# Kernel tuning notes

Hardware: AMD Instinct MI355X
Metric: run time of the kernel (lower is better)

Reference implementation:

```python
import jax, jax.numpy as jnp
import numpy as np

def setup_inputs() -> dict:
    key = jax.random.key(0)
    kS, kD = jax.random.split(key)
    B, Ls, Ld, d = 8, 2048, 2048, 1024
    S = jax.random.normal(kS, (B, Ls, d), dtype=jnp.float32)
    D = jax.random.normal(kD, (B, Ld, d), dtype=jnp.float32)
    return {"S": S, "D": D}

def reference(S, D):
    # scores_D: [B, Ld, Ls] = D @ S^T ; scores_S: [B, Ls, Ld] = S @ D^T
    attn_D = jax.nn.softmax(jnp.einsum('bld,bmd->blm', D, S), axis=-1)
    attn_S = jax.nn.softmax(jnp.einsum('bmd,bld->bml', S, D), axis=-1)
    co_D = D + jnp.einsum('blm,bmd->bld', attn_D, S)
    co_S = S + jnp.einsum('bml,bld->bmd', attn_S, D)
    return (co_D, co_S)
```

## Files before the change

### kernel.cpp

```cpp
#include <hip/hip_runtime.h>

typedef __attribute__((ext_vector_type(8))) _Float16 f16x8;
typedef __attribute__((ext_vector_type(16))) float f32x16;

#define B_    8
#define LSEQ  2048
#define DIM   1024
#define QBLK  64
#define KBLK  128
#define NKB   (LSEQ / KBLK)
#define NDC   (DIM / 128)
#define NBAND (DIM / 128)

#define TILE_US   16384
#define KIMG_US   ((size_t)2 * 8 * 16 * 8 * TILE_US)
#define WS_NEED   ((size_t)2 * KIMG_US * 2)

static __device__ __forceinline__ unsigned pk2(float a, float b) {
    return __builtin_bit_cast(unsigned, __builtin_amdgcn_cvt_pkrtz(a, b));
}

#define VMCNT(n) asm volatile("s_waitcnt vmcnt(" #n ")" ::: "memory")
#define BAR()    do { asm volatile("" ::: "memory"); __builtin_amdgcn_s_barrier(); \
                      asm volatile("" ::: "memory"); } while (0)

static __device__ __forceinline__ void gll16(const void* g, void* l) {
    __builtin_amdgcn_global_load_lds(
        (const __attribute__((address_space(1))) void*)g,
        (__attribute__((address_space(3))) void*)l, 16, 0, 0);
}

static __device__ __forceinline__ void issue32(const unsigned short* gt, unsigned short* lb, int w, int lane) {
    #pragma unroll
    for (int j = 0; j < 4; ++j) {
        const int off = (w * 4 + j) * 1024;
        gll16((const char*)gt + off + lane * 16, (char*)lb + off);
    }
}
static __device__ __forceinline__ void issue16(const unsigned short* gt, unsigned short* lb, int w, int lane) {
    #pragma unroll
    for (int j = 0; j < 2; ++j) {
        const int off = (w * 2 + j) * 1024;
        gll16((const char*)gt + off + lane * 16, (char*)lb + off);
    }
}

__global__ __launch_bounds__(256)
void prepass(const float* __restrict__ Sp, const float* __restrict__ Dp,
             unsigned short* __restrict__ Kimg, unsigned short* __restrict__ Vimg)
{
    const int blk = blockIdx.x;
    const int dc = blk & 7;
    const int kb = (blk >> 3) & 15;
    const int b  = (blk >> 7) & 7;
    const int m  = blk >> 10;
    const float* src = (m ? Dp : Sp) + ((size_t)b * LSEQ + kb * 128) * DIM + dc * 128;
    unsigned short* kt = Kimg + (size_t)((((m * 8 + b) * 16 + kb) * 8) + dc) * TILE_US;
    unsigned short* vt = Vimg + (size_t)((((m * 8 + b) * 8 + dc) * 16) + kb) * TILE_US;

    __shared__ unsigned short tile[128 * 132];
    const int t = threadIdx.x;

    #pragma unroll
    for (int i = 0; i < 16; ++i) {
        const int idx = t + i * 256;
        const int r = idx >> 5;
        const int c4 = (idx & 31) << 2;
        const float4 v = *(const float4*)(src + (size_t)r * DIM + c4);
        const unsigned lo = pk2(v.x, v.y), hi2 = pk2(v.z, v.w);
        *(uint2*)(kt + r * 128 + (c4 ^ ((r & 7) << 3))) = make_uint2(lo, hi2);
        *(uint2*)(&tile[r * 132 + c4]) = make_uint2(lo, hi2);
    }
    __syncthreads();
    #pragma unroll
    for (int i = 0; i < 32; ++i) {
        const int widx = t + i * 256;
        const int dcl = widx >> 6;
        const int wk  = widx & 63;
        const unsigned a  = tile[(wk * 2) * 132 + dcl];
        const unsigned bb = tile[(wk * 2 + 1) * 132 + dcl];
        ((unsigned*)vt)[dcl * 64 + (wk ^ ((dcl & 7) << 2))] = a | (bb << 16);
    }
}

__global__ __launch_bounds__(512, 2)
void coattn_main(const float* __restrict__ Sp, const float* __restrict__ Dp,
                 float* __restrict__ outp,
                 const unsigned short* __restrict__ Kimg,
                 const unsigned short* __restrict__ Vimg)
{
    const int s   = blockIdx.x;
    const int g   = (s & 7) | ((s >> 8) << 3);
    const int qb  = (s >> 3) & 31;
    const int dir = g >> 3;
    const int b   = g & 7;
    const int mat_k = dir;
    const int mat_q = 1 - dir;

    const float* Qg = (dir ? Sp : Dp) + (size_t)b * LSEQ * DIM;
    float* Og = outp + (size_t)dir * ((size_t)B_ * LSEQ * DIM) + (size_t)b * LSEQ * DIM;
    const int q0 = qb * QBLK;

    const unsigned short* kbase = Kimg + (size_t)(mat_k * 8 + b) * 16 * 8 * TILE_US;
    const unsigned short* qbase = Kimg + (size_t)(mat_q * 8 + b) * 16 * 8 * TILE_US
                                + (size_t)(qb >> 1) * 8 * TILE_US + (size_t)(qb & 1) * 8192;
    const unsigned short* vbase = Vimg + (size_t)(mat_k * 8 + b) * 8 * 16 * TILE_US;

    __shared__ unsigned short Rr[3][16384];
    __shared__ unsigned short QR_[3][8192];
    __shared__ float redmax[2][4][32];
    __shared__ float redsum[2][4][32];
    __shared__ float alf[QBLK];

    const int t    = threadIdx.x;
    const int lane = t & 63;
    const int w    = t >> 6;
    const int l31  = lane & 31;
    const int hi   = lane >> 5;
    const int ksub = w & 3;
    const int qh   = w >> 2;

    const int krow = ksub * 32 + l31;
    const int qrow = qh * 32 + l31;
    const int kswz = (krow & 7) << 3;
    const int qswz = (qrow & 7) << 3;
    const int dcl  = ksub * 32 + l31;
    const int vswz = (dcl & 7) << 3;

    unsigned short* Plds = QR_[0];

    f32x16 O[NBAND];
    #pragma unroll
    for (int i = 0; i < NBAND; ++i)
        #pragma unroll
        for (int r = 0; r < 16; ++r) O[i][r] = 0.0f;

    float m_run = -INFINITY, l_run = 0.0f;

    #define QK_MMA(SLOT)                                                          \
    do {                                                                          \
        const unsigned short* Kb = Rr[SLOT];                                      \
        const unsigned short* Qb = QR_[SLOT];                                     \
        __builtin_amdgcn_s_setprio(1);                                            \
        _Pragma("unroll")                                                         \
        for (int kc = 0; kc < 8; ++kc) {                                          \
            const int d0 = kc * 16 + hi * 8;                                      \
            f16x8 a  = *(const f16x8*)&Kb[krow * 128 + (d0 ^ kswz)];              \
            f16x8 bq = *(const f16x8*)&Qb[qrow * 128 + (d0 ^ qswz)];              \
            C = __builtin_amdgcn_mfma_f32_32x32x16_f16(a, bq, C, 0, 0, 0);        \
        }                                                                         \
        __builtin_amdgcn_s_setprio(0);                                            \
    } while (0)

    #define PV_MMA(BAND, SLOT)                                                    \
    do {                                                                          \
        const unsigned short* Vb = Rr[SLOT];                                      \
        __builtin_amdgcn_s_setprio(1);                                            \
        _Pragma("unroll")                                                         \
        for (int kc = 0; kc < 8; ++kc) {                                          \
            const int kk0 = kc * 16 + hi * 8;                                     \
            f16x8 vb = *(const f16x8*)&Vb[dcl * 128 + (kk0 ^ vswz)];              \
            O[BAND] = __builtin_amdgcn_mfma_f32_32x32x16_f16(pa[kc], vb, O[BAND], 0, 0, 0); \
        }                                                                         \
        __builtin_amdgcn_s_setprio(0);                                            \
    } while (0)

    #pragma unroll 1
    for (int kb = 0; kb < NKB; ++kb) {
        const unsigned short* kt = kbase + (size_t)kb * 8 * TILE_US;

        f32x16 C;
        #pragma unroll
        for (int r = 0; r < 16; ++r) C[r] = 0.0f;

        BAR();
        issue32(kt + 0 * TILE_US, Rr[0], w, lane);
        issue16(qbase + 0 * TILE_US, QR_[0], w, lane);
        issue32(kt + 1 * TILE_US, Rr[1], w, lane);
        issue16(qbase + 1 * TILE_US, QR_[1], w, lane);
        VMCNT(6);
        BAR();

        issue32(kt + 2 * TILE_US, Rr[2], w, lane);
        issue16(qbase + 2 * TILE_US, QR_[2], w, lane);
        VMCNT(6);
        QK_MMA(0);

        BAR();
        issue32(kt + 3 * TILE_US, Rr[0], w, lane);
        issue16(qbase + 3 * TILE_US, QR_[0], w, lane);
        VMCNT(6);
        QK_MMA(1);

        BAR();
        issue32(kt + 4 * TILE_US, Rr[1], w, lane);
        issue16(qbase + 4 * TILE_US, QR_[1], w, lane);
        VMCNT(6);
        QK_MMA(2);

        BAR();
        issue32(kt + 5 * TILE_US, Rr[2], w, lane);
        issue16(qbase + 5 * TILE_US, QR_[2], w, lane);
        VMCNT(6);
        QK_MMA(0);

        BAR();
        issue32(kt + 6 * TILE_US, Rr[0], w, lane);
        issue16(qbase + 6 * TILE_US, QR_[0], w, lane);
        VMCNT(6);
        QK_MMA(1);

        BAR();
        issue32(kt + 7 * TILE_US, Rr[1], w, lane);
        issue16(qbase + 7 * TILE_US, QR_[1], w, lane);
        VMCNT(6);
        QK_MMA(2);

        BAR();
        issue32(vbase + (size_t)(0 * 16 + kb) * TILE_US, Rr[2], w, lane);
        VMCNT(4);
        QK_MMA(0);

        BAR();
        issue32(vbase + (size_t)(1 * 16 + kb) * TILE_US, Rr[0], w, lane);
        VMCNT(4);
        QK_MMA(1);

        float rm = -INFINITY;
        #pragma unroll
        for (int r = 0; r < 16; ++r) rm = fmaxf(rm, C[r]);
        rm = fmaxf(rm, __shfl_xor(rm, 32));
        if (lane < 32) redmax[qh][ksub][l31] = rm;
        __syncthreads();

        const float bm = fmaxf(fmaxf(redmax[qh][0][l31], redmax[qh][1][l31]),
                               fmaxf(redmax[qh][2][l31], redmax[qh][3][l31]));
        const float mn = fmaxf(m_run, bm);
        const float al = __expf(m_run - mn);
        float p[16];
        float ps = 0.0f;
        #pragma unroll
        for (int r = 0; r < 16; ++r) { p[r] = __expf(C[r] - mn); ps += p[r]; }
        ps += __shfl_xor(ps, 32);
        if (lane < 32) {
            redsum[qh][ksub][l31] = ps;
            if (ksub == 0) alf[qh * 32 + l31] = al;
        }
        {
            #pragma unroll
            for (int rp = 0; rp < 8; ++rp) {
                const int r  = rp * 2;
                const int kk = ksub * 32 + (r & 3) + 8 * (r >> 2) + 4 * hi;
                *(unsigned*)&Plds[qrow * KBLK + (kk ^ qswz)] = pk2(p[r], p[r + 1]);
            }
        }
        __syncthreads();

        const float bs = redsum[qh][0][l31] + redsum[qh][1][l31] +
                         redsum[qh][2][l31] + redsum[qh][3][l31];
        l_run = l_run * al + bs;
        m_run = mn;

        float alr[16];
        #pragma unroll
        for (int r = 0; r < 16; ++r)
            alr[r] = alf[qh * 32 + (r & 3) + 8 * (r >> 2) + 4 * hi];
        #pragma unroll
        for (int i = 0; i < NBAND; ++i)
            #pragma unroll
            for (int r = 0; r < 16; ++r) O[i][r] *= alr[r];

        f16x8 pa[8];
        #pragma unroll
        for (int kc = 0; kc < 8; ++kc) {
            const int kk0 = kc * 16 + hi * 8;
            pa[kc] = *(const f16x8*)&Plds[qrow * KBLK + (kk0 ^ qswz)];
        }

        issue32(vbase + (size_t)(2 * 16 + kb) * TILE_US, Rr[1], w, lane);
        VMCNT(4);
        PV_MMA(0, 2);

        BAR();
        issue32(vbase + (size_t)(3 * 16 + kb) * TILE_US, Rr[2], w, lane);
        VMCNT(4);
        PV_MMA(1, 0);

        BAR();
        issue32(vbase + (size_t)(4 * 16 + kb) * TILE_US, Rr[0], w, lane);
        VMCNT(4);
        PV_MMA(2, 1);

        BAR();
        issue32(vbase + (size_t)(5 * 16 + kb) * TILE_US, Rr[1], w, lane);
        VMCNT(4);
        PV_MMA(3, 2);

        BAR();
        issue32(vbase + (size_t)(6 * 16 + kb) * TILE_US, Rr[2], w, lane);
        VMCNT(4);
        PV_MMA(4, 0);

        BAR();
        issue32(vbase + (size_t)(7 * 16 + kb) * TILE_US, Rr[0], w, lane);
        VMCNT(4);
        PV_MMA(5, 1);

        BAR();
        PV_MMA(6, 2);

        BAR();
        VMCNT(0);
        PV_MMA(7, 0);
    }

    if (lane < 32 && ksub == 0) alf[qh * 32 + l31] = 1.0f / l_run;
    __syncthreads();
    #pragma unroll
    for (int r = 0; r < 16; ++r) {
        const int qr = qh * 32 + (r & 3) + 8 * (r >> 2) + 4 * hi;
        const float il = alf[qr];
        const size_t rowoff = (size_t)(q0 + qr) * DIM;
        #pragma unroll
        for (int band = 0; band < NBAND; ++band) {
            const int dcol = band * 128 + ksub * 32 + l31;
            Og[rowoff + dcol] = Qg[rowoff + dcol] + O[band][r] * il;
        }
    }
    #undef QK_MMA
    #undef PV_MMA
}

__global__ __launch_bounds__(512, 2)
void coattn_fb(const float* __restrict__ Sp, const float* __restrict__ Dp,
               float* __restrict__ outp)
{
    const int s   = blockIdx.x;
    const int g   = (s & 7) | ((s >> 8) << 3);
    const int qb  = (s >> 3) & 31;
    const int dir = g >> 3;
    const int b   = g & 7;

    const float* Qg = (dir ? Sp : Dp) + (size_t)b * LSEQ * DIM;
    const float* Kg = (dir ? Dp : Sp) + (size_t)b * LSEQ * DIM;
    float* Og = outp + (size_t)dir * ((size_t)B_ * LSEQ * DIM) + (size_t)b * LSEQ * DIM;
    const int q0 = qb * QBLK;

    __shared__ unsigned short Klds[KBLK * 128];
    __shared__ unsigned short Qlds[QBLK * 128];
    __shared__ unsigned short Plds[QBLK * KBLK];
    __shared__ unsigned short Vlds[128 * KBLK];
    __shared__ float redmax[2][4][32];
    __shared__ float redsum[2][4][32];
    __shared__ float alf[QBLK];

    const int t    = threadIdx.x;
    const int lane = t & 63;
    const int w    = t >> 6;
    const int l31  = lane & 31;
    const int hi   = lane >> 5;
    const int ksub = w & 3;
    const int qh   = w >> 2;

    f32x16 O[NBAND];
    #pragma unroll
    for (int i = 0; i < NBAND; ++i)
        #pragma unroll
        for (int r = 0; r < 16; ++r) O[i][r] = 0.0f;

    float m_run = -INFINITY, l_run = 0.0f;

    const int srow = t >> 4;
    const int fcol = (t & 15) << 2;
    const int vmm  = t & 31;
    const int vkp0 = t >> 5;

    const int krow = ksub * 32 + l31;
    const int qrow = qh * 32 + l31;

    for (int kb = 0; kb < NKB; ++kb) {
        const int k0g = kb * KBLK;
        f32x16 C;
        #pragma unroll
        for (int r = 0; r < 16; ++r) C[r] = 0.0f;

        float4 kreg[8], qreg[4];
        #pragma unroll
        for (int pass = 0; pass < 4; ++pass)
            #pragma unroll
            for (int h = 0; h < 2; ++h)
                kreg[pass * 2 + h] = *(const float4*)(Kg + (size_t)(k0g + pass * 32 + srow) * DIM + fcol + h * 64);
        #pragma unroll
        for (int pass = 0; pass < 2; ++pass)
            #pragma unroll
            for (int h = 0; h < 2; ++h)
                qreg[pass * 2 + h] = *(const float4*)(Qg + (size_t)(q0 + pass * 32 + srow) * DIM + fcol + h * 64);

        #pragma unroll 1
        for (int dc = 0; dc < NDC; ++dc) {
            __syncthreads();
            #pragma unroll
            for (int pass = 0; pass < 4; ++pass)
                #pragma unroll
                for (int h = 0; h < 2; ++h) {
                    const int row = pass * 32 + srow;
                    const int d   = fcol + h * 64;
                    const float4 v = kreg[pass * 2 + h];
                    *(uint2*)&Klds[row * 128 + (d ^ ((row & 7) << 3))] =
                        make_uint2(pk2(v.x, v.y), pk2(v.z, v.w));
                }
            #pragma unroll
            for (int pass = 0; pass < 2; ++pass)
                #pragma unroll
                for (int h = 0; h < 2; ++h) {
                    const int row = pass * 32 + srow;
                    const int d   = fcol + h * 64;
                    const float4 v = qreg[pass * 2 + h];
                    *(uint2*)&Qlds[row * 128 + (d ^ ((row & 7) << 3))] =
                        make_uint2(pk2(v.x, v.y), pk2(v.z, v.w));
                }
            __syncthreads();
            if (dc + 1 < NDC) {
                const int dbase = (dc + 1) * 128;
                #pragma unroll
                for (int pass = 0; pass < 4; ++pass)
                    #pragma unroll
                    for (int h = 0; h < 2; ++h)
                        kreg[pass * 2 + h] = *(const float4*)(Kg + (size_t)(k0g + pass * 32 + srow) * DIM + dbase + fcol + h * 64);
                #pragma unroll
                for (int pass = 0; pass < 2; ++pass)
                    #pragma unroll
                    for (int h = 0; h < 2; ++h)
                        qreg[pass * 2 + h] = *(const float4*)(Qg + (size_t)(q0 + pass * 32 + srow) * DIM + dbase + fcol + h * 64);
            }
            #pragma unroll
            for (int kc = 0; kc < 8; ++kc) {
                const int d0 = kc * 16 + hi * 8;
                f16x8 a  = *(const f16x8*)&Klds[krow * 128 + (d0 ^ ((krow & 7) << 3))];
                f16x8 bq = *(const f16x8*)&Qlds[qrow * 128 + (d0 ^ ((qrow & 7) << 3))];
                C = __builtin_amdgcn_mfma_f32_32x32x16_f16(a, bq, C, 0, 0, 0);
            }
        }

        float rm = -INFINITY;
        #pragma unroll
        for (int r = 0; r < 16; ++r) rm = fmaxf(rm, C[r]);
        rm = fmaxf(rm, __shfl_xor(rm, 32));
        if (lane < 32) redmax[qh][ksub][l31] = rm;
        __syncthreads();

        const float bm = fmaxf(fmaxf(redmax[qh][0][l31], redmax[qh][1][l31]),
                               fmaxf(redmax[qh][2][l31], redmax[qh][3][l31]));
        const float mn = fmaxf(m_run, bm);
        const float al = __expf(m_run - mn);
        float p[16];
        float ps = 0.0f;
        #pragma unroll
        for (int r = 0; r < 16; ++r) { p[r] = __expf(C[r] - mn); ps += p[r]; }
        ps += __shfl_xor(ps, 32);
        if (lane < 32) {
            redsum[qh][ksub][l31] = ps;
            if (ksub == 0) alf[qh * 32 + l31] = al;
        }
        {
            #pragma unroll
            for (int rp = 0; rp < 8; ++rp) {
                const int r  = rp * 2;
                const int kk = ksub * 32 + (r & 3) + 8 * (r >> 2) + 4 * hi;
                *(unsigned*)&Plds[qrow * KBLK + (kk ^ ((qrow & 7) << 3))] = pk2(p[r], p[r + 1]);
            }
        }
        __syncthreads();

        const float bs = redsum[qh][0][l31] + redsum[qh][1][l31] +
                         redsum[qh][2][l31] + redsum[qh][3][l31];
        l_run = l_run * al + bs;
        m_run = mn;

        float alr[16];
        #pragma unroll
        for (int r = 0; r < 16; ++r)
            alr[r] = alf[qh * 32 + (r & 3) + 8 * (r >> 2) + 4 * hi];
        #pragma unroll
        for (int i = 0; i < NBAND; ++i)
            #pragma unroll
            for (int r = 0; r < 16; ++r) O[i][r] *= alr[r];

        f16x8 pa[8];
        #pragma unroll
        for (int kc = 0; kc < 8; ++kc) {
            const int kk0 = kc * 16 + hi * 8;
            pa[kc] = *(const f16x8*)&Plds[qrow * KBLK + (kk0 ^ ((qrow & 7) << 3))];
        }

        float4 v0s[4], v1s[4];
        #pragma unroll
        for (int pass = 0; pass < 4; ++pass) {
            const int kp = pass * 16 + vkp0;
            v0s[pass] = *(const float4*)(Kg + (size_t)(k0g + 2 * kp) * DIM + vmm * 4);
            v1s[pass] = *(const float4*)(Kg + (size_t)(k0g + 2 * kp + 1) * DIM + vmm * 4);
        }

        #pragma unroll
        for (int band = 0; band < NBAND; ++band) {
            __syncthreads();
            #pragma unroll
            for (int pass = 0; pass < 4; ++pass) {
                const int kp = pass * 16 + vkp0;
                const float* a0 = (const float*)&v0s[pass];
                const float* a1 = (const float*)&v1s[pass];
                #pragma unroll
                for (int j = 0; j < 4; ++j) {
                    const int dclw = vmm * 4 + j;
                    *(unsigned*)&Vlds[dclw * KBLK + ((2 * kp) ^ ((dclw & 7) << 3))] = pk2(a0[j], a1[j]);
                }
            }
            __syncthreads();
            if (band + 1 < NBAND) {
                const int cb = (band + 1) * 128;
                #pragma unroll
                for (int pass = 0; pass < 4; ++pass) {
                    const int kp = pass * 16 + vkp0;
                    v0s[pass] = *(const float4*)(Kg + (size_t)(k0g + 2 * kp) * DIM + cb + vmm * 4);
                    v1s[pass] = *(const float4*)(Kg + (size_t)(k0g + 2 * kp + 1) * DIM + cb + vmm * 4);
                }
            }
            const int dclr = ksub * 32 + l31;
            const int sw  = (dclr & 7) << 3;
            #pragma unroll
            for (int kc = 0; kc < 8; ++kc) {
                const int kk0 = kc * 16 + hi * 8;
                f16x8 vb = *(const f16x8*)&Vlds[dclr * KBLK + (kk0 ^ sw)];
                O[band] = __builtin_amdgcn_mfma_f32_32x32x16_f16(pa[kc], vb, O[band], 0, 0, 0);
            }
        }
    }

    if (lane < 32 && ksub == 0) alf[qh * 32 + l31] = 1.0f / l_run;
    __syncthreads();
    #pragma unroll
    for (int r = 0; r < 16; ++r) {
        const int qr = qh * 32 + (r & 3) + 8 * (r >> 2) + 4 * hi;
        const float il = alf[qr];
        const size_t rowoff = (size_t)(q0 + qr) * DIM;
        #pragma unroll
        for (int band = 0; band < NBAND; ++band) {
            const int dcol = band * 128 + ksub * 32 + l31;
            Og[rowoff + dcol] = Qg[rowoff + dcol] + O[band][r] * il;
        }
    }
}

extern "C" void kernel_launch(void* const* d_in, const int* in_sizes, int n_in,
                              void* d_out, int out_size, void* d_ws, size_t ws_size,
                              hipStream_t stream) {
    const float* S = (const float*)d_in[0];
    const float* D = (const float*)d_in[1];
    float* out = (float*)d_out;
    if (ws_size >= WS_NEED) {
        unsigned short* Kimg = (unsigned short*)d_ws;
        unsigned short* Vimg = Kimg + KIMG_US;
        prepass<<<dim3(2048, 1, 1), dim3(256, 1, 1), 0, stream>>>(S, D, Kimg, Vimg);
        coattn_main<<<dim3(512, 1, 1), dim3(512, 1, 1), 0, stream>>>(S, D, out, Kimg, Vimg);
    } else {
        coattn_fb<<<dim3(512, 1, 1), dim3(512, 1, 1), 0, stream>>>(S, D, out);
    }
}
```

Baseline: 644.7 us.

## Prefetch next key block's first tiles across iterations with rotating LDS slots

Restructures the LDS ring-buffer pipeline so the first two K/Q tiles of the next key block are issued during the final PV MMAs of the current block. Slot indices now rotate through s3() arithmetic instead of restarting at zero each iteration. This removes the per-iteration pipeline drain and refill bubble. It also swaps __syncthreads for lgkmcnt(0) plus a raw barrier, and moves the barrier ahead of each issue. The cost is more complex slot bookkeeping and a risk of LDS hazards if the rotation is wrong.

```diff
diff --git a/kernel.cpp b/kernel.cpp
--- a/kernel.cpp
+++ b/kernel.cpp
@@ -9,8 +9,7 @@
 #define QBLK  64
 #define KBLK  128
 #define NKB   (LSEQ / KBLK)
-#define NDC   (DIM / 128)
-#define NBAND (DIM / 128)
+#define NBAND 8
 
 #define TILE_US   16384
 #define KIMG_US   ((size_t)2 * 8 * 16 * 8 * TILE_US)
@@ -21,8 +20,11 @@
 }
 
 #define VMCNT(n) asm volatile("s_waitcnt vmcnt(" #n ")" ::: "memory")
+#define LGKM0()  asm volatile("s_waitcnt lgkmcnt(0)" ::: "memory")
 #define BAR()    do { asm volatile("" ::: "memory"); __builtin_amdgcn_s_barrier(); \
                       asm volatile("" ::: "memory"); } while (0)
+
+static __device__ __forceinline__ int s3(int x) { return x >= 3 ? x - 3 : x; }
 
 static __device__ __forceinline__ void gll16(const void* g, void* l) {
     __builtin_amdgcn_global_load_lds(
@@ -127,8 +129,6 @@
     const int dcl  = ksub * 32 + l31;
     const int vswz = (dcl & 7) << 3;
 
-    unsigned short* Plds = QR_[0];
-
     f32x16 O[NBAND];
     #pragma unroll
     for (int i = 0; i < NBAND; ++i)
@@ -137,10 +137,10 @@
 
     float m_run = -INFINITY, l_run = 0.0f;
 
-    #define QK_MMA(SLOT)                                                          \
+    #define QK_MMA(RS, QS)                                                        \
     do {                                                                          \
-        const unsigned short* Kb = Rr[SLOT];                                      \
-        const unsigned short* Qb = QR_[SLOT];                                     \
+        const unsigned short* Kb = Rr[RS];                                        \
+        const unsigned short* Qb = QR_[QS];                                       \
         __builtin_amdgcn_s_setprio(1);                                            \
         _Pragma("unroll")                                                         \
         for (int kc = 0; kc < 8; ++kc) {                                          \
@@ -152,9 +152,9 @@
         __builtin_amdgcn_s_setprio(0);                                            \
     } while (0)
 
-    #define PV_MMA(BAND, SLOT)                                                    \
+    #define PV_MMA(BAND, RS)                                                      \
     do {                                                                          \
-        const unsigned short* Vb = Rr[SLOT];                                      \
+        const unsigned short* Vb = Rr[RS];                                        \
         __builtin_amdgcn_s_setprio(1);                                            \
         _Pragma("unroll")                                                         \
         for (int kc = 0; kc < 8; ++kc) {                                          \
@@ -165,6 +165,32 @@
         __builtin_amdgcn_s_setprio(0);                                            \
     } while (0)
 
+    #define QK_PHASE(P)                                                           \
+    do {                                                                          \
+        VMCNT(6); BAR();                                                          \
+        issue32(kt + (P + 2) * TILE_US, Rr[s3(sb + ((P + 2) % 3))], w, lane);     \
+        issue16(qbase + (P + 2) * TILE_US, QR_[s3(qsb + ((P + 2) % 3))], w, lane);\
+        QK_MMA(s3(sb + (P % 3)), s3(qsb + (P % 3)));                              \
+    } while (0)
+
+    #define PV_PHASE(V)                                                           \
+    do {                                                                          \
+        VMCNT(4); BAR();                                                          \
+        issue32(vbase + (size_t)((V + 2) * 16 + kb) * TILE_US,                    \
+                Rr[s3(sb + ((V + 10) % 3))], w, lane);                            \
+        PV_MMA(V, s3(sb + ((V + 8) % 3)));                                        \
+    } while (0)
+
+    {
+        const unsigned short* kt0 = kbase;
+        issue32(kt0 + 0 * TILE_US, Rr[0], w, lane);
+        issue16(qbase + 0 * TILE_US, QR_[0], w, lane);
+        issue32(kt0 + 1 * TILE_US, Rr[1], w, lane);
+        issue16(qbase + 1 * TILE_US, QR_[1], w, lane);
+    }
+
+    int sb = 0, qsb = 0;
+
     #pragma unroll 1
     for (int kb = 0; kb < NKB; ++kb) {
         const unsigned short* kt = kbase + (size_t)kb * 8 * TILE_US;
@@ -173,65 +199,23 @@
         #pragma unroll
         for (int r = 0; r < 16; ++r) C[r] = 0.0f;
 
-        BAR();
-        issue32(kt + 0 * TILE_US, Rr[0], w, lane);
-        issue16(qbase + 0 * TILE_US, QR_[0], w, lane);
-        issue32(kt + 1 * TILE_US, Rr[1], w, lane);
-        issue16(qbase + 1 * TILE_US, QR_[1], w, lane);
-        VMCNT(6);
-        BAR();
-
-        issue32(kt + 2 * TILE_US, Rr[2], w, lane);
-        issue16(qbase + 2 * TILE_US, QR_[2], w, lane);
-        VMCNT(6);
-        QK_MMA(0);
-
-        BAR();
-        issue32(kt + 3 * TILE_US, Rr[0], w, lane);
-        issue16(qbase + 3 * TILE_US, QR_[0], w, lane);
-        VMCNT(6);
-        QK_MMA(1);
-
-        BAR();
-        issue32(kt + 4 * TILE_US, Rr[1], w, lane);
-        issue16(qbase + 4 * TILE_US, QR_[1], w, lane);
-        VMCNT(6);
-        QK_MMA(2);
-
-        BAR();
-        issue32(kt + 5 * TILE_US, Rr[2], w, lane);
-        issue16(qbase + 5 * TILE_US, QR_[2], w, lane);
-        VMCNT(6);
-        QK_MMA(0);
-
-        BAR();
-        issue32(kt + 6 * TILE_US, Rr[0], w, lane);
-        issue16(qbase + 6 * TILE_US, QR_[0], w, lane);
-        VMCNT(6);
-        QK_MMA(1);
-
-        BAR();
-        issue32(kt + 7 * TILE_US, Rr[1], w, lane);
-        issue16(qbase + 7 * TILE_US, QR_[1], w, lane);
-        VMCNT(6);
-        QK_MMA(2);
-
-        BAR();
-        issue32(vbase + (size_t)(0 * 16 + kb) * TILE_US, Rr[2], w, lane);
-        VMCNT(4);
-        QK_MMA(0);
-
-        BAR();
-        issue32(vbase + (size_t)(1 * 16 + kb) * TILE_US, Rr[0], w, lane);
-        VMCNT(4);
-        QK_MMA(1);
+        QK_PHASE(0); QK_PHASE(1); QK_PHASE(2);
+        QK_PHASE(3); QK_PHASE(4); QK_PHASE(5);
+        VMCNT(6); BAR();
+        issue32(vbase + (size_t)(0 * 16 + kb) * TILE_US, Rr[s3(sb + 2)], w, lane);
+        QK_MMA(s3(sb + 0), s3(qsb + 0));
+        VMCNT(4); BAR();
+        issue32(vbase + (size_t)(1 * 16 + kb) * TILE_US, Rr[s3(sb + 0)], w, lane);
+        QK_MMA(s3(sb + 1), s3(qsb + 1));
+
+        unsigned short* Plds = QR_[s3(qsb + 1)];
 
         float rm = -INFINITY;
         #pragma unroll
         for (int r = 0; r < 16; ++r) rm = fmaxf(rm, C[r]);
         rm = fmaxf(rm, __shfl_xor(rm, 32));
         if (lane < 32) redmax[qh][ksub][l31] = rm;
-        __syncthreads();
+        LGKM0(); BAR();
 
         const float bm = fmaxf(fmaxf(redmax[qh][0][l31], redmax[qh][1][l31]),
                                fmaxf(redmax[qh][2][l31], redmax[qh][3][l31]));
@@ -254,7 +238,7 @@
                 *(unsigned*)&Plds[qrow * KBLK + (kk ^ qswz)] = pk2(p[r], p[r + 1]);
             }
         }
-        __syncthreads();
+        LGKM0(); BAR();
 
         const float bs = redsum[qh][0][l31] + redsum[qh][1][l31] +
                          redsum[qh][2][l31] + redsum[qh][3][l31];
@@ -277,43 +261,30 @@
             pa[kc] = *(const f16x8*)&Plds[qrow * KBLK + (kk0 ^ qswz)];
         }
 
-        issue32(vbase + (size_t)(2 * 16 + kb) * TILE_US, Rr[1], w, lane);
-        VMCNT(4);
-        PV_MMA(0, 2);
-
-        BAR();
-        issue32(vbase + (size_t)(3 * 16 + kb) * TILE_US, Rr[2], w, lane);
-        VMCNT(4);
-        PV_MMA(1, 0);
-
-        BAR();
-        issue32(vbase + (size_t)(4 * 16 + kb) * TILE_US, Rr[0], w, lane);
-        VMCNT(4);
-        PV_MMA(2, 1);
-
-        BAR();
-        issue32(vbase + (size_t)(5 * 16 + kb) * TILE_US, Rr[1], w, lane);
-        VMCNT(4);
-        PV_MMA(3, 2);
-
-        BAR();
-        issue32(vbase + (size_t)(6 * 16 + kb) * TILE_US, Rr[2], w, lane);
-        VMCNT(4);
-        PV_MMA(4, 0);
-
-        BAR();
-        issue32(vbase + (size_t)(7 * 16 + kb) * TILE_US, Rr[0], w, lane);
-        VMCNT(4);
-        PV_MMA(5, 1);
-
-        BAR();
-        PV_MMA(6, 2);
-
-        BAR();
-        VMCNT(0);
-        PV_MMA(7, 0);
-    }
-
+        PV_PHASE(0); PV_PHASE(1); PV_PHASE(2);
+        PV_PHASE(3); PV_PHASE(4); PV_PHASE(5);
+        VMCNT(4); BAR();
+        if (kb + 1 < NKB) {
+            const unsigned short* ktn = kbase + (size_t)(kb + 1) * 8 * TILE_US;
+            issue32(ktn + 0 * TILE_US, Rr[s3(sb + 1)], w, lane);
+            issue16(qbase + 0 * TILE_US, QR_[s3(qsb + 2)], w, lane);
+        }
+        PV_MMA(6, s3(sb + 2));
+        if (kb + 1 < NKB) {
+            VMCNT(6); BAR();
+            const unsigned short* ktn = kbase + (size_t)(kb + 1) * 8 * TILE_US;
+            issue32(ktn + 1 * TILE_US, Rr[s3(sb + 2)], w, lane);
+            issue16(qbase + 1 * TILE_US, QR_[qsb], w, lane);
+        } else {
+            VMCNT(0); BAR();
+        }
+        PV_MMA(7, sb);
+
+        sb = s3(sb + 1);
+        qsb = s3(qsb + 2);
+    }
+
+    __syncthreads();
     if (lane < 32 && ksub == 0) alf[qh * 32 + l31] = 1.0f / l_run;
     __syncthreads();
     #pragma unroll
@@ -329,7 +300,11 @@
     }
     #undef QK_MMA
     #undef PV_MMA
-}
+    #undef QK_PHASE
+    #undef PV_PHASE
+}
+
+#define NDC   8
 
 __global__ __launch_bounds__(512, 2)
 void coattn_fb(const float* __restrict__ Sp, const float* __restrict__ Dp,
```

Result: slower. 869.5 us (+34.9%).
